# Kernel tuning notes

Measured on AMD Instinct MI355X. Metric: run time of the kernel, lower is better.

## Reference

```python
import jax, jax.numpy as jnp
import numpy as np

K = 1024   # num_embeddings
E = 64     # embedding_dim
T = 1024   # time
B = 64     # batch
BETA = 0.25  # commitment_cost


def setup_inputs() -> dict:
    key = jax.random.key(0)
    k1, k2 = jax.random.split(key)
    inputs = jax.random.normal(k1, (E, T, B), dtype=jnp.float32)
    # torch init: uniform(-1/num_embeddings, 1/num_embeddings)
    codebook = jax.random.uniform(k2, (K, E), dtype=jnp.float32,
                                  minval=-1.0 / K, maxval=1.0 / K)
    return {"inputs": inputs, "codebook": codebook}


def reference(inputs, codebook):
    # inputs: [E, T, B]; torch does permute(1,2,0) -> [T, B, E]
    x = jnp.transpose(inputs, (1, 2, 0))            # [T, B, E]
    flat = x.reshape(-1, E)                          # [N, E], N = T*B
    d = (jnp.sum(flat * flat, axis=1, keepdims=True)
         + jnp.sum(codebook * codebook, axis=1)
         - 2.0 * (flat @ codebook.T))
    idx = jnp.argmin(d, axis=1)                      # [N]
    # one-hot @ codebook == gather (same math, efficient form)
    q = codebook[idx].reshape(T, B, E)               # [T, B, E]

    e_latent_loss = jnp.mean((jax.lax.stop_gradient(q) - x) ** 2)
    q_latent_loss = jnp.mean((q - jax.lax.stop_gradient(x)) ** 2)
    vq_loss = q_latent_loss + BETA * e_latent_loss

    # straight-through estimator
    q_st = x + jax.lax.stop_gradient(q - x)

    # perplexity from code-usage histogram (mean of one-hots)
    N = flat.shape[0]
    counts = jnp.zeros((K,), jnp.float32).at[idx].add(1.0)
    avg_probs = counts / N
    perplexity = jnp.exp(-jnp.sum(avg_probs * jnp.log(avg_probs + 1e-10)))

    quantized = jnp.transpose(q_st, (2, 0, 1))       # back to [E, T, B]
    return vq_loss, quantized, perplexity
```

## Files before the change

### kernel.cpp

```cpp
#include <hip/hip_runtime.h>


#define KC 1024
#define ED 64
#define NR 65536
#define NE (NR * ED)
#define GAP1 6e-6f

typedef __attribute__((ext_vector_type(8))) short short8;
typedef __attribute__((ext_vector_type(4))) float f32x4;

__device__ __forceinline__ unsigned short bf16rne(float f) {
    unsigned u = __builtin_bit_cast(unsigned, f);
    return (unsigned short)((u + 0x7fffu + ((u >> 16) & 1u)) >> 16);
}
__device__ __forceinline__ float bf16tof(unsigned short h) {
    return __builtin_bit_cast(float, (unsigned)h << 16);
}

__global__ __launch_bounds__(256) void k_pack(const float* __restrict__ cb,
        short8* __restrict__ cbt, unsigned* __restrict__ counts,
        unsigned* __restrict__ flagcnt) {
    const int u = blockIdx.x * 256 + threadIdx.x;
    if (u < 1024) counts[u] = 0u;
    if (u == 1024) *flagcnt = 0u;
    if (u >= 64 * 5 * 64) return;
    const int t = u / 320, rem = u % 320, j = rem / 64, l = rem % 64;
    const int g = l >> 4;
    if (j < 4) {
        const int code = t * 16 + (l & 15);
        const float* c = cb + (size_t)code * ED;
        const bool lo = (j >= 2);
        short8 o;
#pragma unroll
        for (int r = 0; r < 8; ++r) {
            const int e = (j & 1) * 32 + g * 8 + r;
            const float m2 = -2.f * c[e];
            const unsigned short h = bf16rne(m2);
            o[r] = lo ? (short)bf16rne(m2 - bf16tof(h)) : (short)h;
        }
        cbt[u] = o;
    } else {
        f32x4 o;
#pragma unroll
        for (int r = 0; r < 4; ++r) {
            const float4* c4 = (const float4*)(cb + (size_t)(t * 16 + g * 4 + r) * ED);
            float s0 = 0.f, s1 = 0.f, s2 = 0.f, s3 = 0.f;
#pragma unroll
            for (int i = 0; i < 16; ++i) {
                const float4 c = c4[i];
                s0 = fmaf(c.x, c.x, s0); s1 = fmaf(c.y, c.y, s1);
                s2 = fmaf(c.z, c.z, s2); s3 = fmaf(c.w, c.w, s3);
            }
            o[r] = (s0 + s1) + (s2 + s3);
        }
        cbt[u] = __builtin_bit_cast(short8, o);
    }
}

__global__ __launch_bounds__(1024) void k_argmin(
        const float* __restrict__ in, const short8* __restrict__ cbt,
        int* __restrict__ idx, unsigned* __restrict__ counts,
        unsigned* __restrict__ flagcnt, unsigned* __restrict__ flaglist,
        double* __restrict__ pblk) {
    __shared__ short8 xs[4][16][64];
    __shared__ float rx2p[4][256];
    __shared__ float sb[16][4][16], sb2[16][4][16];
    __shared__ int   sk[16][4][16];
    __shared__ double sred[4];

    const int tid = threadIdx.x;
    const int l = tid & 63;
    const int wid = tid >> 6;
    const int g = l >> 4;
    const int col = l & 15;
    const int rowBase = blockIdx.x * 256;

    {
        const int row = tid & 255;
        const int ob = tid >> 8;
        const int rg = row >> 6;
        const int r6 = row & 63;
        const int rt = r6 >> 4;
        const int ll = ob * 16 + (r6 & 15);
        float part = 0.f;
#pragma unroll
        for (int hh = 0; hh < 2; ++hh) {
            const int oct = ob + hh * 4;
            short8 H, L;
#pragma unroll
            for (int j = 0; j < 8; ++j) {
                const float x = in[(size_t)(oct * 8 + j) * NR + rowBase + row];
                const unsigned short hb = bf16rne(x);
                H[j] = (short)hb;
                L[j] = (short)bf16rne(x - bf16tof(hb));
                part = fmaf(x, x, part);
            }
            xs[rg][rt * 4 + hh][ll] = H;
            xs[rg][rt * 4 + 2 + hh][ll] = L;
        }
        rx2p[ob][row] = part;
    }
    __syncthreads();

    const int rg = wid >> 2, kh = wid & 3;
    short8 xq[4][4];
#pragma unroll
    for (int rt = 0; rt < 4; ++rt)
#pragma unroll
        for (int q = 0; q < 4; ++q)
            xq[rt][q] = xs[rg][rt * 4 + q][l];

    float best[4]  = {3.4e38f, 3.4e38f, 3.4e38f, 3.4e38f};
    float best2[4] = {3.4e38f, 3.4e38f, 3.4e38f, 3.4e38f};
    int bestk[4] = {0, 0, 0, 0};

#pragma unroll 2
    for (int tt = 0; tt < 16; ++tt) {
        const int t = kh * 16 + tt;
        const short8* bp = cbt + (size_t)t * 320 + l;
        const short8 b0 = bp[0], b1 = bp[64], b2 = bp[128], b3 = bp[192];
        const f32x4 e4 = __builtin_bit_cast(f32x4, bp[256]);
#pragma unroll
        for (int rt = 0; rt < 4; ++rt) {
            f32x4 acc = e4;
            acc = __builtin_amdgcn_mfma_f32_16x16x32_bf16(b0, xq[rt][0], acc, 0, 0, 0);
            acc = __builtin_amdgcn_mfma_f32_16x16x32_bf16(b1, xq[rt][1], acc, 0, 0, 0);
            acc = __builtin_amdgcn_mfma_f32_16x16x32_bf16(b2, xq[rt][0], acc, 0, 0, 0);
            acc = __builtin_amdgcn_mfma_f32_16x16x32_bf16(b3, xq[rt][1], acc, 0, 0, 0);
            acc = __builtin_amdgcn_mfma_f32_16x16x32_bf16(b0, xq[rt][2], acc, 0, 0, 0);
            acc = __builtin_amdgcn_mfma_f32_16x16x32_bf16(b1, xq[rt][3], acc, 0, 0, 0);
#pragma unroll
            for (int r = 0; r < 4; ++r) {
                const float v = acc[r];
                const int k = t * 16 + g * 4 + r;
                best2[rt] = fminf(fmaxf(v, best[rt]), best2[rt]);
                const bool c = v < best[rt];
                bestk[rt] = c ? k : bestk[rt];
                best[rt]  = fminf(v, best[rt]);
            }
        }
    }

#pragma unroll
    for (int rt = 0; rt < 4; ++rt) {
        float b = best[rt], b2 = best2[rt]; int k = bestk[rt];
#pragma unroll
        for (int sh = 16; sh <= 32; sh <<= 1) {
            const float ob  = __shfl_xor(b, sh, 64);
            const float ob2 = __shfl_xor(b2, sh, 64);
            const int   ok  = __shfl_xor(k, sh, 64);
            if (ob < b || (ob == b && ok < k)) { b2 = fminf(b, ob2); k = ok; b = ob; }
            else b2 = fminf(b2, ob);
        }
        if (g == 0) { sb[wid][rt][col] = b; sb2[wid][rt][col] = b2; sk[wid][rt][col] = k; }
    }
    __syncthreads();

    if (wid < 4) {
        const int rt = l >> 4, c2 = l & 15;
        float b = sb[wid * 4][rt][c2], b2 = sb2[wid * 4][rt][c2];
        int k = sk[wid * 4][rt][c2];
#pragma unroll
        for (int s = 1; s < 4; ++s) {
            const float ob = sb[wid * 4 + s][rt][c2], ob2 = sb2[wid * 4 + s][rt][c2];
            const int ok = sk[wid * 4 + s][rt][c2];
            if (ob < b || (ob == b && ok < k)) { b2 = fminf(b, ob2); k = ok; b = ob; }
            else b2 = fminf(b2, ob);
        }
        const int lrow = wid * 64 + rt * 16 + c2;
        const int row = rowBase + lrow;
        idx[row] = k;
        atomicAdd(&counts[k], 1u);
        if (b2 - b < GAP1) {
            const unsigned p = atomicAdd(flagcnt, 1u);
            flaglist[p] = (unsigned)row;
        }
        double d2 = (double)b + (double)((rx2p[0][lrow] + rx2p[1][lrow])
                                       + (rx2p[2][lrow] + rx2p[3][lrow]));
#pragma unroll
        for (int off = 32; off > 0; off >>= 1) d2 += __shfl_down(d2, off, 64);
        if (l == 0) sred[wid] = d2;
    }
    __syncthreads();
    if (tid == 0)
        pblk[blockIdx.x] = (sred[0] + sred[1]) + (sred[2] + sred[3]);
}

__global__ __launch_bounds__(256) void k_exact64(
        const float* __restrict__ in, const float* __restrict__ cb,
        int* __restrict__ idx, unsigned* __restrict__ counts,
        const unsigned* __restrict__ flagcnt, const unsigned* __restrict__ flaglist) {
    const unsigned nf = *flagcnt;
    const int l = threadIdx.x & 63;
    const unsigned wave = blockIdx.x * 4u + (unsigned)(threadIdx.x >> 6);
    const unsigned nwave = gridDim.x * 4u;
    for (unsigned i = wave; i < nf; i += nwave) {
        const int row = (int)flaglist[i];
        float x[ED];
#pragma unroll
        for (int e = 0; e < ED; ++e) x[e] = in[(size_t)e * NR + row];
        double best = 1e300; int bestk = 0;
        for (int ci = 0; ci < 16; ++ci) {
            const int k = ci * 64 + l;
            const float* c = cb + (size_t)k * ED;
            double s = 0.0, e2 = 0.0;
            for (int e = 0; e < ED; ++e) {
                const double cv = (double)c[e];
                e2 = fma(cv, cv, e2);
                s  = fma(cv, (double)x[e], s);
            }
            const double t = fma(-2.0, s, e2);
            if (t < best) { best = t; bestk = k; }
        }
        for (int sh = 1; sh < 64; sh <<= 1) {
            const double ob = __shfl_xor(best, sh, 64);
            const int   ok  = __shfl_xor(bestk, sh, 64);
            if (ob < best || (ob == best && ok < bestk)) { best = ob; bestk = ok; }
        }
        if (l == 0) {
            const int old = idx[row];
            if (bestk != old) {
                idx[row] = bestk;
                atomicSub(&counts[old], 1u);
                atomicAdd(&counts[bestk], 1u);
            }
        }
    }
}

__global__ __launch_bounds__(256) void k_output(
        const float* __restrict__ cb, const int* __restrict__ idx,
        float* __restrict__ qout, const unsigned* __restrict__ counts,
        const double* __restrict__ pblk, float* __restrict__ out) {
    const int gtid = blockIdx.x * 256 + threadIdx.x;
    const int n = gtid & (NR - 1);
    const int e0 = gtid >> 16;
    const int k = idx[n];
    const float4* c4 = (const float4*)(cb + (size_t)k * ED + e0 * 8);
    const float4 q0 = c4[0], q1 = c4[1];
#pragma unroll
    for (int j = 0; j < 8; ++j) {
        const float q = (j < 4) ? ((const float*)&q0)[j] : ((const float*)&q1)[j - 4];
        qout[(size_t)(e0 * 8 + j) * NR + n] = q;
    }
    if (blockIdx.x == 0) {
        __shared__ double redE[4], redS[4];
        const int tid = threadIdx.x;
        double term = 0.0;
#pragma unroll
        for (int i = 0; i < 4; ++i) {
            const double p = (double)counts[tid + i * 256] * (1.0 / 65536.0);
            term += p * log(p + 1e-10);
        }
        double s = pblk[tid];
#pragma unroll
        for (int off = 32; off > 0; off >>= 1) {
            term += __shfl_down(term, off, 64);
            s    += __shfl_down(s,    off, 64);
        }
        if ((tid & 63) == 0) { redE[tid >> 6] = term; redS[tid >> 6] = s; }
        __syncthreads();
        if (tid == 0) {
            const double e = (redE[0] + redE[1]) + (redE[2] + redE[3]);
            const double ss = (redS[0] + redS[1]) + (redS[2] + redS[3]);
            out[1 + NE] = (float)exp(-e);
            const double m = ss * (1.0 / 4194304.0);
            out[0] = (float)(1.25 * m);
        }
    }
}

extern "C" void kernel_launch(void* const* d_in, const int* in_sizes, int n_in,
                              void* d_out, int out_size, void* d_ws, size_t ws_size,
                              hipStream_t stream) {
    (void)in_sizes; (void)n_in; (void)out_size; (void)ws_size;
    const float* in = (const float*)d_in[0];
    const float* cb = (const float*)d_in[1];
    float* out = (float*)d_out;

    unsigned* counts   = (unsigned*)d_ws;
    unsigned* flagcnt  = (unsigned*)d_ws + 1024;
    short8*   cbt      = (short8*)((float*)d_ws + 2048);
    int*      idx      = (int*)d_ws + 83968;
    unsigned* flaglist = (unsigned*)d_ws + 149504;
    double*   pblk     = (double*)((char*)d_ws + 991232);

    hipLaunchKernelGGL(k_pack,    dim3(80),   dim3(256),  0, stream,
                       cb, cbt, counts, flagcnt);
    hipLaunchKernelGGL(k_argmin,  dim3(256),  dim3(1024), 0, stream,
                       in, cbt, idx, counts, flagcnt, flaglist, pblk);
    hipLaunchKernelGGL(k_exact64, dim3(128),  dim3(256),  0, stream,
                       in, cb, idx, counts, flagcnt, flaglist);
    hipLaunchKernelGGL(k_output,  dim3(2048), dim3(256),  0, stream,
                       cb, idx, out + 1, counts, pblk, out);
}
```

Before: 86.24 us.

## Fuse quantized-output gather into argmin kernel and halve rows per block

The separate output kernel, which reread idx and gathered codebook rows, is folded into the argmin kernel. Each block now writes its own quantized columns from a shared-memory index cache. Blocks shrink to 512 threads covering 128 rows, doubling the grid. The exact-refinement kernel rewrites the quantized output for rows whose index changes, and a tiny single-block kernel does the loss and perplexity reductions. This removes one full pass over idx and a launch, but adds scattered column writes to the argmin kernel and changes occupancy.

```diff
diff --git a/kernel.cpp b/kernel.cpp
--- a/kernel.cpp
+++ b/kernel.cpp
@@ -58,27 +58,29 @@
     }
 }
 
-__global__ __launch_bounds__(1024) void k_argmin(
+__global__ __launch_bounds__(512) void k_argmin(
         const float* __restrict__ in, const short8* __restrict__ cbt,
-        int* __restrict__ idx, unsigned* __restrict__ counts,
+        const float* __restrict__ cb, int* __restrict__ idx,
+        float* __restrict__ qout, unsigned* __restrict__ counts,
         unsigned* __restrict__ flagcnt, unsigned* __restrict__ flaglist,
         double* __restrict__ pblk) {
-    __shared__ short8 xs[4][16][64];
-    __shared__ float rx2p[4][256];
-    __shared__ float sb[16][4][16], sb2[16][4][16];
-    __shared__ int   sk[16][4][16];
-    __shared__ double sred[4];
+    __shared__ short8 xs[2][16][64];
+    __shared__ float rx2p[4][128];
+    __shared__ float sb[8][4][16], sb2[8][4][16];
+    __shared__ int   sk[8][4][16];
+    __shared__ int   fidx[128];
+    __shared__ double sred[2];
 
     const int tid = threadIdx.x;
     const int l = tid & 63;
     const int wid = tid >> 6;
     const int g = l >> 4;
     const int col = l & 15;
-    const int rowBase = blockIdx.x * 256;
+    const int rowBase = blockIdx.x * 128;
 
     {
-        const int row = tid & 255;
-        const int ob = tid >> 8;
+        const int row = tid & 127;
+        const int ob = tid >> 7;
         const int rg = row >> 6;
         const int r6 = row & 63;
         const int rt = r6 >> 4;
@@ -157,7 +159,7 @@
     }
     __syncthreads();
 
-    if (wid < 4) {
+    if (wid < 2) {
         const int rt = l >> 4, c2 = l & 15;
         float b = sb[wid * 4][rt][c2], b2 = sb2[wid * 4][rt][c2];
         int k = sk[wid * 4][rt][c2];
@@ -171,6 +173,7 @@
         const int lrow = wid * 64 + rt * 16 + c2;
         const int row = rowBase + lrow;
         idx[row] = k;
+        fidx[lrow] = k;
         atomicAdd(&counts[k], 1u);
         if (b2 - b < GAP1) {
             const unsigned p = atomicAdd(flagcnt, 1u);
@@ -183,13 +186,28 @@
         if (l == 0) sred[wid] = d2;
     }
     __syncthreads();
-    if (tid == 0)
-        pblk[blockIdx.x] = (sred[0] + sred[1]) + (sred[2] + sred[3]);
+    if (tid == 0) pblk[blockIdx.x] = sred[0] + sred[1];
+
+    {
+        const int row = tid & 127;
+        const int e0 = tid >> 7;
+        const int k = fidx[row];
+        const float4* c4 = (const float4*)(cb + (size_t)k * ED + e0 * 16);
+#pragma unroll
+        for (int j = 0; j < 4; ++j) {
+            const float4 v = c4[j];
+            qout[(size_t)(e0 * 16 + j * 4 + 0) * NR + rowBase + row] = v.x;
+            qout[(size_t)(e0 * 16 + j * 4 + 1) * NR + rowBase + row] = v.y;
+            qout[(size_t)(e0 * 16 + j * 4 + 2) * NR + rowBase + row] = v.z;
+            qout[(size_t)(e0 * 16 + j * 4 + 3) * NR + rowBase + row] = v.w;
+        }
+    }
 }
 
 __global__ __launch_bounds__(256) void k_exact64(
         const float* __restrict__ in, const float* __restrict__ cb,
-        int* __restrict__ idx, unsigned* __restrict__ counts,
+        int* __restrict__ idx, float* __restrict__ qout,
+        unsigned* __restrict__ counts,
         const unsigned* __restrict__ flagcnt, const unsigned* __restrict__ flaglist) {
     const unsigned nf = *flagcnt;
     const int l = threadIdx.x & 63;
@@ -218,56 +236,38 @@
             const int   ok  = __shfl_xor(bestk, sh, 64);
             if (ob < best || (ob == best && ok < bestk)) { best = ob; bestk = ok; }
         }
-        if (l == 0) {
-            const int old = idx[row];
-            if (bestk != old) {
+        const int old = idx[row];
+        if (bestk != old) {
+            if (l == 0) {
                 idx[row] = bestk;
                 atomicSub(&counts[old], 1u);
                 atomicAdd(&counts[bestk], 1u);
             }
-        }
-    }
-}
-
-__global__ __launch_bounds__(256) void k_output(
-        const float* __restrict__ cb, const int* __restrict__ idx,
-        float* __restrict__ qout, const unsigned* __restrict__ counts,
+            qout[(size_t)l * NR + row] = cb[(size_t)bestk * ED + l];
+        }
+    }
+}
+
+__global__ __launch_bounds__(1024) void k_final(const unsigned* __restrict__ counts,
         const double* __restrict__ pblk, float* __restrict__ out) {
-    const int gtid = blockIdx.x * 256 + threadIdx.x;
-    const int n = gtid & (NR - 1);
-    const int e0 = gtid >> 16;
-    const int k = idx[n];
-    const float4* c4 = (const float4*)(cb + (size_t)k * ED + e0 * 8);
-    const float4 q0 = c4[0], q1 = c4[1];
-#pragma unroll
-    for (int j = 0; j < 8; ++j) {
-        const float q = (j < 4) ? ((const float*)&q0)[j] : ((const float*)&q1)[j - 4];
-        qout[(size_t)(e0 * 8 + j) * NR + n] = q;
-    }
-    if (blockIdx.x == 0) {
-        __shared__ double redE[4], redS[4];
-        const int tid = threadIdx.x;
-        double term = 0.0;
-#pragma unroll
-        for (int i = 0; i < 4; ++i) {
-            const double p = (double)counts[tid + i * 256] * (1.0 / 65536.0);
-            term += p * log(p + 1e-10);
-        }
-        double s = pblk[tid];
-#pragma unroll
-        for (int off = 32; off > 0; off >>= 1) {
-            term += __shfl_down(term, off, 64);
-            s    += __shfl_down(s,    off, 64);
-        }
-        if ((tid & 63) == 0) { redE[tid >> 6] = term; redS[tid >> 6] = s; }
-        __syncthreads();
-        if (tid == 0) {
-            const double e = (redE[0] + redE[1]) + (redE[2] + redE[3]);
-            const double ss = (redS[0] + redS[1]) + (redS[2] + redS[3]);
-            out[1 + NE] = (float)exp(-e);
-            const double m = ss * (1.0 / 4194304.0);
-            out[0] = (float)(1.25 * m);
-        }
+    __shared__ double redE[16], redS[16];
+    const int tid = threadIdx.x;
+    const double p = (double)counts[tid] * (1.0 / 65536.0);
+    double term = p * log(p + 1e-10);
+    double s = (tid < 512) ? pblk[tid] : 0.0;
+#pragma unroll
+    for (int off = 32; off > 0; off >>= 1) {
+        term += __shfl_down(term, off, 64);
+        s    += __shfl_down(s,    off, 64);
+    }
+    if ((tid & 63) == 0) { redE[tid >> 6] = term; redS[tid >> 6] = s; }
+    __syncthreads();
+    if (tid == 0) {
+        double e = 0.0, ss = 0.0;
+        for (int i = 0; i < 16; ++i) { e += redE[i]; ss += redS[i]; }
+        out[1 + NE] = (float)exp(-e);
+        const double m = ss * (1.0 / 4194304.0);
+        out[0] = (float)(1.25 * m);
     }
 }
 
@@ -286,12 +286,12 @@
     unsigned* flaglist = (unsigned*)d_ws + 149504;
     double*   pblk     = (double*)((char*)d_ws + 991232);
 
-    hipLaunchKernelGGL(k_pack,    dim3(80),   dim3(256),  0, stream,
+    hipLaunchKernelGGL(k_pack,    dim3(80),  dim3(256),  0, stream,
                        cb, cbt, counts, flagcnt);
-    hipLaunchKernelGGL(k_argmin,  dim3(256),  dim3(1024), 0, stream,
-                       in, cbt, idx, counts, flagcnt, flaglist, pblk);
-    hipLaunchKernelGGL(k_exact64, dim3(128),  dim3(256),  0, stream,
-                       in, cb, idx, counts, flagcnt, flaglist);
-    hipLaunchKernelGGL(k_output,  dim3(2048), dim3(256),  0, stream,
-                       cb, idx, out + 1, counts, pblk, out);
-}
+    hipLaunchKernelGGL(k_argmin,  dim3(512), dim3(512),  0, stream,
+                       in, cbt, cb, idx, out + 1, counts, flagcnt, flaglist, pblk);
+    hipLaunchKernelGGL(k_exact64, dim3(128), dim3(256),  0, stream,
+                       in, cb, idx, out + 1, counts, flagcnt, flaglist);
+    hipLaunchKernelGGL(k_final,   dim3(1),   dim3(1024), 0, stream,
+                       counts, pblk, out);
+}
```

After: 81.25 us. 1.06x faster.
